# Optimization experiments

Measured on AMD Instinct MI355X. Metric: run time of the kernel, lower is better.

Reference implementation:

```python
import jax, jax.numpy as jnp
import numpy as np

FS = 3          # filter_size
B, C, H, W = 16, 256, 96, 96
BN_EPS = 1e-5


def setup_inputs() -> dict:
    key = jax.random.key(0)
    ks = jax.random.split(key, 6)
    s = 0.05
    return {
        "x": jax.random.normal(ks[0], (B, C, H, W), jnp.float32),
        "convoluted": jax.random.normal(ks[1], (B, C, H, W), jnp.float32),
        # filter_gen_conv: 1x1 Conv2d(C -> C)
        "w_gen": jax.random.normal(ks[2], (C, C, 1, 1), jnp.float32) * s,
        "b_gen": jax.random.normal(ks[3], (C,), jnp.float32) * s,
        # c1: 3x3 Conv2d(C -> C) + BatchNorm2d(C) + ReLU
        "w_c1": jax.random.normal(ks[4], (C, C, 3, 3), jnp.float32) * s,
        "b_c1": jax.random.normal(ks[5], (C,), jnp.float32) * s,
        "gamma": jnp.ones((C,), jnp.float32),
        "beta": jnp.zeros((C,), jnp.float32),
    }


def reference(x, convoluted, w_gen, b_gen, w_c1, b_c1, gamma, beta):
    b, c, h, w = x.shape
    # adaptive_avg_pool2d(x, FS): H,W divisible by FS -> uniform bins
    pooled = x.reshape(b, c, FS, h // FS, FS, w // FS).mean(axis=(3, 5))  # [b,c,FS,FS]
    # 1x1 conv generating per-sample per-channel filters
    gen = jnp.einsum('bcij,oc->boij', pooled, w_gen[:, :, 0, 0]) + b_gen[None, :, None, None]

    # c1: conv3x3 (pad 1) + BatchNorm (training-mode batch stats) + ReLU
    y = jax.lax.conv_general_dilated(
        convoluted, w_c1, window_strides=(1, 1), padding=((1, 1), (1, 1)),
        dimension_numbers=('NCHW', 'OIHW', 'NCHW')) + b_c1[None, :, None, None]
    mu = y.mean(axis=(0, 2, 3), keepdims=True)
    var = y.var(axis=(0, 2, 3), keepdims=True)
    y = (y - mu) * jax.lax.rsqrt(var + BN_EPS)
    y = jax.nn.relu(y * gamma[None, :, None, None] + beta[None, :, None, None])

    # dynamic per-sample depthwise conv: groups = b*c, symmetric pad (FS odd)
    y = y.reshape(1, b * c, h, w)
    filt = gen.reshape(b * c, 1, FS, FS)
    pad = (FS - 1) // 2
    out = jax.lax.conv_general_dilated(
        y, filt, window_strides=(1, 1), padding=((pad, pad), (pad, pad)),
        feature_group_count=b * c, dimension_numbers=('NCHW', 'OIHW', 'NCHW'))
    return out.reshape(b, c, h, w)
```

## Files before the change

kernel.cpp:

```cpp
#include <hip/hip_runtime.h>

typedef __bf16 bf16x8 __attribute__((ext_vector_type(8)));
typedef float f32x4 __attribute__((ext_vector_type(4)));

static __device__ __forceinline__ ushort f2b(float f) {
    uint32_t x = __float_as_uint(f);
    x += 0x7fffu + ((x >> 16) & 1u);
    return (ushort)(x >> 16);
}
static __device__ __forceinline__ float b2f(ushort u) {
    return __uint_as_float(((uint32_t)u) << 16);
}

typedef const __attribute__((address_space(1))) uint32_t gu32;
typedef __attribute__((address_space(3))) uint32_t lu32;
static __device__ __forceinline__ void gl_lds16(const void* g, void* l) {
    __builtin_amdgcn_global_load_lds((gu32*)g, (lu32*)l, 16, 0, 0);
}

__global__ __launch_bounds__(256) void pool_k(const float* __restrict__ x,
                                              float* __restrict__ pooled) {
    const int bc  = blockIdx.x;
    const int tid = threadIdx.x;
    const int lane = tid & 63, wv = tid >> 6;
    const float4* p4 = (const float4*)(x + (size_t)bc * 9216);
    __shared__ float red[4][9];
#pragma unroll
    for (int bi = 0; bi < 3; ++bi) {
#pragma unroll
        for (int bj = 0; bj < 3; ++bj) {
            int row = bi * 32 + (tid >> 3);
            int c4  = bj * 8 + (tid & 7);
            float4 f = p4[row * 24 + c4];
            float s = f.x + f.y + f.z + f.w;
#pragma unroll
            for (int off = 32; off; off >>= 1) s += __shfl_down(s, off);
            if (lane == 0) red[wv][bi * 3 + bj] = s;
        }
    }
    __syncthreads();
    if (tid < 9) {
        float s = red[0][tid] + red[1][tid] + red[2][tid] + red[3][tid];
        pooled[(size_t)bc * 9 + tid] = s * (1.0f / 1024.0f);
    }
}

__global__ __launch_bounds__(256) void gen_k(const float* __restrict__ pooled,
                                             const float* __restrict__ wgen,
                                             const float* __restrict__ bgen,
                                             float* __restrict__ gen) {
    __shared__ float pl[256];
    const int b = blockIdx.x / 9, ij = blockIdx.x % 9;
    const int o = threadIdx.x;
    pl[o] = pooled[((size_t)b * 256 + o) * 9 + ij];
    __syncthreads();
    float a = bgen[o];
    const float4* wg4 = (const float4*)(wgen + (size_t)o * 256);
    const float4* pl4 = (const float4*)pl;
#pragma unroll 4
    for (int q = 0; q < 64; ++q) {
        float4 w = wg4[q], p = pl4[q];
        a += w.x * p.x + w.y * p.y + w.z * p.z + w.w * p.w;
    }
    gen[((size_t)b * 256 + o) * 9 + ij] = a;
}

__global__ __launch_bounds__(256) void wtr_k(const float* __restrict__ wc1,
                                             ushort* __restrict__ wtr) {
    int g = blockIdx.x * 256 + threadIdx.x;
    int step = g >> 10;
    int row  = (g >> 2) & 255;
    int c8   = g & 3;
    int ch = step / 9, tap = step - ch * 9;
    int cb = ch * 32 + c8 * 8;
    ushort tmp[8];
#pragma unroll
    for (int j = 0; j < 8; ++j)
        tmp[j] = f2b(wc1[(size_t)row * 2304 + (size_t)(cb + j) * 9 + tap]);
    *(uint4*)(wtr + (size_t)g * 8) = *(const uint4*)tmp;
}

__global__ __launch_bounds__(512) void xt_k(const float* __restrict__ xin,
                                            ushort* __restrict__ xt,
                                            ushort* __restrict__ zeros) {
    __shared__ ushort T[96][258];
    const int bh = blockIdx.x;
    const int b = bh / 96, h = bh % 96;
    const int tid = threadIdx.x;
    const float* src = xin + (size_t)b * 2359296 + (size_t)h * 96;
#pragma unroll
    for (int it = 0; it < 12; ++it) {
        int id = tid + it * 512;
        int c = id / 24, q = id - c * 24;
        float4 v = *(const float4*)(src + (size_t)c * 9216 + q * 4);
        int px = q * 4;
        T[px + 0][c] = f2b(v.x); T[px + 1][c] = f2b(v.y);
        T[px + 2][c] = f2b(v.z); T[px + 3][c] = f2b(v.w);
    }
    __syncthreads();
    ushort* dst = xt + (size_t)bh * 24576;
#pragma unroll
    for (int it = 0; it < 12; ++it) {
        int id = tid + it * 512;
        int px = id >> 6, cq = id & 63;
        ushort4 u;
        u.x = T[px][cq * 4 + 0]; u.y = T[px][cq * 4 + 1];
        u.z = T[px][cq * 4 + 2]; u.w = T[px][cq * 4 + 3];
        *(ushort4*)(dst + px * 256 + cq * 4) = u;
    }
    if (bh == 0) {
        uint4 zz; zz.x = zz.y = zz.z = zz.w = 0u;
        *(uint4*)(zeros + (size_t)tid * 8) = zz;
    }
}

__global__ __launch_bounds__(256, 3) void conv_k(const ushort* __restrict__ xt,
                                                 const ushort* __restrict__ wtr,
                                                 const float* __restrict__ bc1,
                                                 const ushort* __restrict__ zeros,
                                                 ushort* __restrict__ yb,
                                                 float* __restrict__ part) {
    __shared__ ushort Bl[2][9408];

    const int blk0 = blockIdx.x;
    const int blk = (blk0 & 7) * 384 + (blk0 >> 3);
    const int ohalf = blk & 1, rowblk = blk >> 1;
    const int b = rowblk / 96, h = rowblk % 96;
    const int tid = threadIdx.x;
    const int lane = tid & 63, wv = tid >> 6;
    const int wm = wv >> 1, wn = wv & 1;
    const int lo = lane & 15, hi = lane >> 4;

#pragma unroll
    for (int z0 = 0; z0 < 2; ++z0) {
        int z = tid + z0 * 256;
        if (z < 384) {
            int bsel = z >= 192, rem = z - bsel * 192;
            int row = rem >> 6, pxp = ((rem >> 5) & 1) ? 97 : 0, c = rem & 31;
            Bl[bsel][(row * 98 + pxp) * 32 + c] = 0;
        }
    }

    const int laneoff = (lane >> 2) * 256 + (lane & 3) * 8;

    auto stage = [&](int chunk, int buf) {
#pragma unroll
        for (int j = 0; j < 5; ++j) {
            const int s = wv + j * 4;
            if (s < 18) {
                const int row = s / 6, pseg = s - (s / 6) * 6;
                const int r = h + row - 1;
                const ushort* base = ((unsigned)r < 96u)
                    ? (xt + ((size_t)(b * 96 + r) * 96 + pseg * 16) * 256
                          + chunk * 32)
                    : zeros;
                gl_lds16(base + laneoff,
                         &Bl[buf][(row * 98 + 1 + pseg * 16) * 32]);
            }
        }
    };

    const uint4* Abase =
        (const uint4*)wtr + ((ohalf * 128 + wm * 64 + lo) * 4 + hi);

    f32x4 acc[4][3] = {};
    uint4 abuf[3][4];

    stage(0, 0);
#pragma unroll
    for (int mi = 0; mi < 4; ++mi) abuf[0][mi] = Abase[mi * 64];
#pragma unroll
    for (int mi = 0; mi < 4; ++mi) abuf[1][mi] = (Abase + 1024)[mi * 64];
    __syncthreads();

    for (int k = 0; k < 4; ++k) {
#pragma unroll
        for (int t = 0; t < 18; ++t) {
            if (t == 0) stage(2 * k + 1, 1);
            else if (t == 9 && k < 3) stage(2 * k + 2, 0);
            if (t < 16 || k < 3) {
                const uint4* Ap = Abase + (size_t)(k * 18 + t + 2) * 1024;
#pragma unroll
                for (int mi = 0; mi < 4; ++mi)
                    abuf[(t + 2) % 3][mi] = Ap[mi * 64];
            }
            const int tap = (t < 9) ? t : t - 9;
            const int dy = tap / 3, dx = tap % 3;
            const ushort* Bp =
                &Bl[t >= 9][(dy * 98 + wn * 48 + lo + dx) * 32 + hi * 8];
            bf16x8 bfr[3];
#pragma unroll
            for (int ni = 0; ni < 3; ++ni)
                bfr[ni] = *(const bf16x8*)(Bp + ni * 512);
#pragma unroll
            for (int mi = 0; mi < 4; ++mi) {
                const bf16x8 af = *(const bf16x8*)&abuf[t % 3][mi];
#pragma unroll
                for (int ni = 0; ni < 3; ++ni)
                    acc[mi][ni] = __builtin_amdgcn_mfma_f32_16x16x32_bf16(
                        af, bfr[ni], acc[mi][ni], 0, 0, 0);
            }
            if (t == 8) __syncthreads();
            else if (t == 17 && k < 3) __syncthreads();
        }
    }

    const size_t ybase = (size_t)rowblk * 24576;
    float* red = (float*)&Bl[0][0];
    __syncthreads();
#pragma unroll
    for (int mi = 0; mi < 4; ++mi) {
        float s[4], s2[4];
#pragma unroll
        for (int rr = 0; rr < 4; ++rr) {
            const int o = ohalf * 128 + wm * 64 + mi * 16 + hi * 4 + rr;
            const float bias = bc1[o];
            float sv = 0.f, sv2 = 0.f;
#pragma unroll
            for (int ni = 0; ni < 3; ++ni) {
                const int px = wn * 48 + ni * 16 + lo;
                float v = acc[mi][ni][rr] + bias;
                yb[ybase + o * 96 + px] = f2b(v);
                sv += v; sv2 += v * v;
            }
            s[rr] = sv; s2[rr] = sv2;
        }
#pragma unroll
        for (int off = 1; off < 16; off <<= 1) {
#pragma unroll
            for (int rr = 0; rr < 4; ++rr) {
                s[rr]  += __shfl_xor(s[rr], off);
                s2[rr] += __shfl_xor(s2[rr], off);
            }
        }
        if (lo == 0) {
#pragma unroll
            for (int rr = 0; rr < 4; ++rr) {
                const int ol = wm * 64 + mi * 16 + hi * 4 + rr;
                red[ol * 4 + wn * 2 + 0] = s[rr];
                red[ol * 4 + wn * 2 + 1] = s2[rr];
            }
        }
    }
    __syncthreads();
    if (tid < 128) {
        const int o = ohalf * 128 + tid;
        part[(size_t)o * 1536 + rowblk]          = red[tid * 4] + red[tid * 4 + 2];
        part[393216 + (size_t)o * 1536 + rowblk] = red[tid * 4 + 1] + red[tid * 4 + 3];
    }
}

__global__ __launch_bounds__(256) void bnred_k(const float* __restrict__ part,
                                               const float* __restrict__ gamma,
                                               const float* __restrict__ beta,
                                               float* __restrict__ bnp) {
    const int o = blockIdx.x, t = threadIdx.x;
    const float* p0 = part + (size_t)o * 1536;
    const float* p1 = p0 + 393216;
    float s = 0.f, s2 = 0.f;
#pragma unroll
    for (int k = 0; k < 6; ++k) { s += p0[t + k * 256]; s2 += p1[t + k * 256]; }
    const int lane = t & 63, wv = t >> 6;
#pragma unroll
    for (int off = 32; off; off >>= 1) {
        s  += __shfl_down(s, off);
        s2 += __shfl_down(s2, off);
    }
    __shared__ float r1[4], r2[4];
    if (lane == 0) { r1[wv] = s; r2[wv] = s2; }
    __syncthreads();
    if (t == 0) {
        float S  = r1[0] + r1[1] + r1[2] + r1[3];
        float S2 = r2[0] + r2[1] + r2[2] + r2[3];
        const float invN = 1.0f / 147456.0f;
        float mu  = S * invN;
        float var = S2 * invN - mu * mu;
        float sc  = gamma[o] * rsqrtf(var + 1e-5f);
        bnp[o]       = sc;
        bnp[256 + o] = beta[o] - mu * sc;
    }
}

__global__ __launch_bounds__(256) void dw_k(const ushort* __restrict__ yb,
                                            const float* __restrict__ gen,
                                            const float* __restrict__ bnp,
                                            float* __restrict__ out) {
    __shared__ float pl[98][104];
    const int bc = blockIdx.x, tid = threadIdx.x;
    const int b = bc >> 8, c = bc & 255;
    const float sc = bnp[c], sh = bnp[256 + c];

#pragma unroll
    for (int z0 = 0; z0 < 4; ++z0) {
        int z = tid + z0 * 256;
        if (z < 104) pl[0][z] = 0.f;
        else if (z < 208) pl[97][z - 104] = 0.f;
        else if (z < 976) {
            int w = z - 208;
            int r = (w >> 3) + 1, j = w & 7;
            pl[r][(j < 4) ? j : 96 + j] = 0.f;
        }
    }

    const ushort4* yb4 = (const ushort4*)yb;
    const size_t pbase = (size_t)b * 589824 + c * 24;
#pragma unroll
    for (int it = 0; it < 9; ++it) {
        int e4 = tid + it * 256;
        int row = e4 / 24, q = e4 - row * 24;
        ushort4 u = yb4[pbase + (size_t)row * 6144 + q];
        float4 f;
        f.x = fmaxf(b2f(u.x) * sc + sh, 0.f);
        f.y = fmaxf(b2f(u.y) * sc + sh, 0.f);
        f.z = fmaxf(b2f(u.z) * sc + sh, 0.f);
        f.w = fmaxf(b2f(u.w) * sc + sh, 0.f);
        *(float4*)&pl[row + 1][q * 4 + 4] = f;
    }
    float g[9];
    const float* gp = gen + (size_t)bc * 9;
#pragma unroll
    for (int k = 0; k < 9; ++k) g[k] = gp[k];
    __syncthreads();

    float4* op4 = (float4*)(out + (size_t)bc * 9216);
#pragma unroll
    for (int it = 0; it < 9; ++it) {
        int e4 = tid + it * 256;
        int row = e4 / 24, q = e4 - row * 24;
        float4 o4 = {0.f, 0.f, 0.f, 0.f};
#pragma unroll
        for (int dy = 0; dy < 3; ++dy) {
            const float4* pr = (const float4*)&pl[row + dy][0];
            float4 x0 = pr[q];
            float4 x1 = pr[q + 1];
            float4 x2 = pr[q + 2];
            const float w0 = g[dy * 3 + 0], w1 = g[dy * 3 + 1],
                        w2 = g[dy * 3 + 2];
            o4.x += w0 * x0.w + w1 * x1.x + w2 * x1.y;
            o4.y += w0 * x1.x + w1 * x1.y + w2 * x1.z;
            o4.z += w0 * x1.y + w1 * x1.z + w2 * x1.w;
            o4.w += w0 * x1.z + w1 * x1.w + w2 * x2.x;
        }
        op4[e4] = o4;
    }
}

extern "C" void kernel_launch(void* const* d_in, const int* in_sizes, int n_in,
                              void* d_out, int out_size, void* d_ws, size_t ws_size,
                              hipStream_t stream) {
    const float* x       = (const float*)d_in[0];
    const float* conv_in = (const float*)d_in[1];
    const float* w_gen   = (const float*)d_in[2];
    const float* b_gen   = (const float*)d_in[3];
    const float* w_c1    = (const float*)d_in[4];
    const float* b_c1    = (const float*)d_in[5];
    const float* gamma   = (const float*)d_in[6];
    const float* beta    = (const float*)d_in[7];
    float* out = (float*)d_out;

    char* ws = (char*)d_ws;
    float*  pooled = (float*)(ws + 0);
    float*  gen    = (float*)(ws + 147456);
    ushort* wtr    = (ushort*)(ws + 294912);
    float*  part   = (float*)(ws + 1474560);
    float*  bnp    = (float*)(ws + 4620288);
    ushort* zeros  = (ushort*)(ws + 4622336);
    ushort* yb     = (ushort*)(ws + 4630528);
    ushort* xt     = (ushort*)d_out;

    pool_k <<<4096, 256, 0, stream>>>(x, pooled);
    gen_k  <<<144,  256, 0, stream>>>(pooled, w_gen, b_gen, gen);
    wtr_k  <<<288,  256, 0, stream>>>(w_c1, wtr);
    xt_k   <<<1536, 512, 0, stream>>>(conv_in, xt, zeros);
    conv_k <<<3072, 256, 0, stream>>>(xt, wtr, b_c1, zeros, yb, part);
    bnred_k<<<256,  256, 0, stream>>>(part, gamma, beta, bnp);
    dw_k   <<<4096, 256, 0, stream>>>(yb, gen, bnp, out);
}
```

Before: 376.7 us.

## Switch conv3x3 to 32x32x16 MFMA with full-channel tiles per block

The conv kernel moves from 16x16x32 to 32x32x16 bf16 MFMA tiles. Each block now covers all 256 output channels of one image row instead of half, so the launch shrinks to 1536 blocks and the staged input row is reused across twice as many channels. The weight pre-transpose is re-laid out to match the new A-fragment pattern, and the BN partial reduction is rewritten for the 32-lane accumulator layout. The larger accumulator set raises register pressure, so occupancy drops to 2 blocks per CU, and fewer blocks means coarser load balance.

```diff
diff --git a/kernel.cpp b/kernel.cpp
--- a/kernel.cpp
+++ b/kernel.cpp
@@ -2,6 +2,7 @@
 
 typedef __bf16 bf16x8 __attribute__((ext_vector_type(8)));
 typedef float f32x4 __attribute__((ext_vector_type(4)));
+typedef float f32x16 __attribute__((ext_vector_type(16)));
 
 static __device__ __forceinline__ ushort f2b(float f) {
     uint32_t x = __float_as_uint(f);
@@ -69,14 +70,17 @@
                                              ushort* __restrict__ wtr) {
     int g = blockIdx.x * 256 + threadIdx.x;
     int step = g >> 10;
-    int row  = (g >> 2) & 255;
-    int c8   = g & 3;
+    int rem  = g & 1023;
+    int grp  = rem >> 6;
+    int l    = rem & 63;
+    int t32 = grp >> 1, ks = grp & 1;
     int ch = step / 9, tap = step - ch * 9;
-    int cb = ch * 32 + c8 * 8;
+    int o  = t32 * 32 + (l & 31);
+    int cb = ch * 32 + ks * 16 + (l >> 5) * 8;
     ushort tmp[8];
 #pragma unroll
     for (int j = 0; j < 8; ++j)
-        tmp[j] = f2b(wc1[(size_t)row * 2304 + (size_t)(cb + j) * 9 + tap]);
+        tmp[j] = f2b(wc1[(size_t)o * 2304 + (size_t)(cb + j) * 9 + tap]);
     *(uint4*)(wtr + (size_t)g * 8) = *(const uint4*)tmp;
 }
 
@@ -114,7 +118,7 @@
     }
 }
 
-__global__ __launch_bounds__(256, 3) void conv_k(const ushort* __restrict__ xt,
+__global__ __launch_bounds__(256, 2) void conv_k(const ushort* __restrict__ xt,
                                                  const ushort* __restrict__ wtr,
                                                  const float* __restrict__ bc1,
                                                  const ushort* __restrict__ zeros,
@@ -123,13 +127,11 @@
     __shared__ ushort Bl[2][9408];
 
     const int blk0 = blockIdx.x;
-    const int blk = (blk0 & 7) * 384 + (blk0 >> 3);
-    const int ohalf = blk & 1, rowblk = blk >> 1;
-    const int b = rowblk / 96, h = rowblk % 96;
+    const int blk = (blk0 & 7) * 192 + (blk0 >> 3);
+    const int b = blk / 96, h = blk % 96;
     const int tid = threadIdx.x;
     const int lane = tid & 63, wv = tid >> 6;
-    const int wm = wv >> 1, wn = wv & 1;
-    const int lo = lane & 15, hi = lane >> 4;
+    const int l31 = lane & 31, lh = lane >> 5;
 
 #pragma unroll
     for (int z0 = 0; z0 < 2; ++z0) {
@@ -160,17 +162,16 @@
         }
     };
 
-    const uint4* Abase =
-        (const uint4*)wtr + ((ohalf * 128 + wm * 64 + lo) * 4 + hi);
-
-    f32x4 acc[4][3] = {};
+    const uint4* Abase = (const uint4*)wtr + wv * 256 + lane;
+
+    f32x16 acc[2][3] = {};
     uint4 abuf[3][4];
 
     stage(0, 0);
 #pragma unroll
-    for (int mi = 0; mi < 4; ++mi) abuf[0][mi] = Abase[mi * 64];
-#pragma unroll
-    for (int mi = 0; mi < 4; ++mi) abuf[1][mi] = (Abase + 1024)[mi * 64];
+    for (int f = 0; f < 4; ++f) abuf[0][f] = Abase[f * 64];
+#pragma unroll
+    for (int f = 0; f < 4; ++f) abuf[1][f] = Abase[1024 + f * 64];
     __syncthreads();
 
     for (int k = 0; k < 4; ++k) {
@@ -181,72 +182,77 @@
             if (t < 16 || k < 3) {
                 const uint4* Ap = Abase + (size_t)(k * 18 + t + 2) * 1024;
 #pragma unroll
-                for (int mi = 0; mi < 4; ++mi)
-                    abuf[(t + 2) % 3][mi] = Ap[mi * 64];
+                for (int f = 0; f < 4; ++f)
+                    abuf[(t + 2) % 3][f] = Ap[f * 64];
             }
             const int tap = (t < 9) ? t : t - 9;
             const int dy = tap / 3, dx = tap % 3;
             const ushort* Bp =
-                &Bl[t >= 9][(dy * 98 + wn * 48 + lo + dx) * 32 + hi * 8];
-            bf16x8 bfr[3];
+                &Bl[t >= 9][(dy * 98 + l31 + dx) * 32 + lh * 8];
+            bf16x8 bfr[3][2];
 #pragma unroll
             for (int ni = 0; ni < 3; ++ni)
-                bfr[ni] = *(const bf16x8*)(Bp + ni * 512);
-#pragma unroll
-            for (int mi = 0; mi < 4; ++mi) {
-                const bf16x8 af = *(const bf16x8*)&abuf[t % 3][mi];
-#pragma unroll
-                for (int ni = 0; ni < 3; ++ni)
-                    acc[mi][ni] = __builtin_amdgcn_mfma_f32_16x16x32_bf16(
-                        af, bfr[ni], acc[mi][ni], 0, 0, 0);
-            }
+#pragma unroll
+                for (int ks = 0; ks < 2; ++ks)
+                    bfr[ni][ks] = *(const bf16x8*)(Bp + ni * 1024 + ks * 16);
+#pragma unroll
+            for (int ks = 0; ks < 2; ++ks)
+#pragma unroll
+                for (int mi = 0; mi < 2; ++mi) {
+                    const bf16x8 af =
+                        *(const bf16x8*)&abuf[t % 3][mi * 2 + ks];
+#pragma unroll
+                    for (int ni = 0; ni < 3; ++ni)
+                        acc[mi][ni] = __builtin_amdgcn_mfma_f32_32x32x16_bf16(
+                            af, bfr[ni][ks], acc[mi][ni], 0, 0, 0);
+                }
             if (t == 8) __syncthreads();
             else if (t == 17 && k < 3) __syncthreads();
         }
     }
 
-    const size_t ybase = (size_t)rowblk * 24576;
+    const size_t ybase = (size_t)blk * 24576;
     float* red = (float*)&Bl[0][0];
     __syncthreads();
 #pragma unroll
-    for (int mi = 0; mi < 4; ++mi) {
-        float s[4], s2[4];
-#pragma unroll
-        for (int rr = 0; rr < 4; ++rr) {
-            const int o = ohalf * 128 + wm * 64 + mi * 16 + hi * 4 + rr;
+    for (int mi = 0; mi < 2; ++mi) {
+        const int ob = wv * 64 + mi * 32;
+        float s[16], s2[16];
+#pragma unroll
+        for (int r = 0; r < 16; ++r) {
+            const int o = ob + (r & 3) + 8 * (r >> 2) + 4 * lh;
             const float bias = bc1[o];
             float sv = 0.f, sv2 = 0.f;
 #pragma unroll
             for (int ni = 0; ni < 3; ++ni) {
-                const int px = wn * 48 + ni * 16 + lo;
-                float v = acc[mi][ni][rr] + bias;
-                yb[ybase + o * 96 + px] = f2b(v);
+                float v = acc[mi][ni][r] + bias;
+                yb[ybase + o * 96 + ni * 32 + l31] = f2b(v);
                 sv += v; sv2 += v * v;
             }
-            s[rr] = sv; s2[rr] = sv2;
-        }
-#pragma unroll
-        for (int off = 1; off < 16; off <<= 1) {
-#pragma unroll
-            for (int rr = 0; rr < 4; ++rr) {
-                s[rr]  += __shfl_xor(s[rr], off);
-                s2[rr] += __shfl_xor(s2[rr], off);
-            }
-        }
-        if (lo == 0) {
-#pragma unroll
-            for (int rr = 0; rr < 4; ++rr) {
-                const int ol = wm * 64 + mi * 16 + hi * 4 + rr;
-                red[ol * 4 + wn * 2 + 0] = s[rr];
-                red[ol * 4 + wn * 2 + 1] = s2[rr];
-            }
-        }
-    }
-    __syncthreads();
-    if (tid < 128) {
-        const int o = ohalf * 128 + tid;
-        part[(size_t)o * 1536 + rowblk]          = red[tid * 4] + red[tid * 4 + 2];
-        part[393216 + (size_t)o * 1536 + rowblk] = red[tid * 4 + 1] + red[tid * 4 + 3];
+            s[r] = sv; s2[r] = sv2;
+        }
+#pragma unroll
+        for (int off = 1; off < 32; off <<= 1) {
+#pragma unroll
+            for (int r = 0; r < 16; ++r) {
+                s[r]  += __shfl_xor(s[r], off);
+                s2[r] += __shfl_xor(s2[r], off);
+            }
+        }
+        if (l31 == 0) {
+#pragma unroll
+            for (int r = 0; r < 16; ++r) {
+                const int ol = ob + (r & 3) + 8 * (r >> 2) + 4 * lh;
+                red[ol * 2]     = s[r];
+                red[ol * 2 + 1] = s2[r];
+            }
+        }
+    }
+    __syncthreads();
+    {
+        const int o = tid;
+        part[(size_t)o * 1536 + blk]          = red[o * 2];
+        part[393216 + (size_t)o * 1536 + blk] = red[o * 2 + 1];
     }
 }
 
@@ -372,7 +378,7 @@
     gen_k  <<<144,  256, 0, stream>>>(pooled, w_gen, b_gen, gen);
     wtr_k  <<<288,  256, 0, stream>>>(w_c1, wtr);
     xt_k   <<<1536, 512, 0, stream>>>(conv_in, xt, zeros);
-    conv_k <<<3072, 256, 0, stream>>>(xt, wtr, b_c1, zeros, yb, part);
+    conv_k <<<1536, 256, 0, stream>>>(xt, wtr, b_c1, zeros, yb, part);
     bnred_k<<<256,  256, 0, stream>>>(part, gamma, beta, bnp);
     dw_k   <<<4096, 256, 0, stream>>>(yb, gen, bnp, out);
 }
```

Result: faster. 328.9 us (-12.7%).
